# Performance work log

Hardware: AMD Instinct MI355X
Metric: run time of the kernel (lower is better)

Reference implementation:

```python
import jax, jax.numpy as jnp
import numpy as np

N_HEADS = 16
N_KV = 4
HEAD_DIM = 256
EPS = 1e-6

def _rotate_half(x):
    h = x.shape[-1] // 2
    return jnp.concatenate([-x[..., h:], x[..., :h]], axis=-1)

def _gemma_rmsnorm(x, w, eps=EPS):
    dt = x.dtype
    x32 = x.astype(jnp.float32)
    x32 = x32 * jax.lax.rsqrt(jnp.mean(x32 * x32, axis=-1, keepdims=True) + eps)
    return ((1.0 + w.astype(jnp.float32)) * x32).astype(dt)


def setup_inputs() -> dict:
    key = jax.random.key(0)
    ks = jax.random.split(key, 7)
    B, S, D = 2, 2048, 4096
    rotary_dim = 64
    x = jax.random.normal(ks[0], (B, S, D), jnp.float32)
    # realistic RoPE cache: [cos | sin], theta=10000
    inv_freq = 1.0 / (10000.0 ** (np.arange(0, rotary_dim, 2, dtype=np.float32) / rotary_dim))
    t = np.arange(S, dtype=np.float32)
    freqs = np.outer(t, inv_freq)                       # [S, rotary_dim/2]
    emb = np.concatenate([freqs, freqs], axis=-1)        # [S, rotary_dim]
    rope_cache = jnp.asarray(np.concatenate([np.cos(emb), np.sin(emb)], axis=-1))  # [S, 2*rotary_dim]
    sc = 0.02
    wq = jax.random.normal(ks[1], (N_HEADS * HEAD_DIM * 2, D), jnp.float32) * sc
    wk = jax.random.normal(ks[2], (N_KV * HEAD_DIM, D), jnp.float32) * sc
    wv = jax.random.normal(ks[3], (N_KV * HEAD_DIM, D), jnp.float32) * sc
    wo = jax.random.normal(ks[4], (D, N_HEADS * HEAD_DIM), jnp.float32) * sc
    q_norm_w = jnp.zeros((HEAD_DIM,), jnp.float32)
    k_norm_w = jnp.zeros((HEAD_DIM,), jnp.float32)
    return {"x": x, "rope_cache": rope_cache, "wq": wq, "wk": wk, "wv": wv,
            "wo": wo, "q_norm_w": q_norm_w, "k_norm_w": k_norm_w}


def reference(x, rope_cache, wq, wk, wv, wo, q_norm_w, k_norm_w):
    B, S, D = x.shape
    scale = HEAD_DIM ** -0.5
    # fused QKV-style projections
    qg = jnp.einsum('bsd,ed->bse', x, wq).reshape(B, S, N_HEADS, 2 * HEAD_DIM)
    q, gate = qg[..., :HEAD_DIM], qg[..., HEAD_DIM:]
    gate = gate.reshape(B, S, N_HEADS * HEAD_DIM)
    k = jnp.einsum('bsd,ed->bse', x, wk).reshape(B, S, N_KV, HEAD_DIM)
    v = jnp.einsum('bsd,ed->bse', x, wv).reshape(B, S, N_KV, HEAD_DIM)
    # QK RMSNorm (Gemma-style, zero-init weight)
    q = _gemma_rmsnorm(q, q_norm_w)
    k = _gemma_rmsnorm(k, k_norm_w)
    # partial RoPE on first rotary_dim dims
    rotary_dim = rope_cache.shape[-1] // 2
    rc = rope_cache[:S]
    cos = rc[None, :, None, :rotary_dim]
    sin = rc[None, :, None, rotary_dim:]
    q_rot = q[..., :rotary_dim] * cos + _rotate_half(q[..., :rotary_dim]) * sin
    k_rot = k[..., :rotary_dim] * cos + _rotate_half(k[..., :rotary_dim]) * sin
    q = jnp.concatenate([q_rot, q[..., rotary_dim:]], axis=-1)
    k = jnp.concatenate([k_rot, k[..., rotary_dim:]], axis=-1)
    # GQA: repeat kv heads
    rep = N_HEADS // N_KV
    k = jnp.repeat(k, rep, axis=2)  # [B,S,H,hd]
    v = jnp.repeat(v, rep, axis=2)
    # full (non-causal) SDPA
    scores = jnp.einsum('bqhd,bkhd->bhqk', q, k) * scale
    p = jax.nn.softmax(scores, axis=-1)
    y = jnp.einsum('bhqk,bkhd->bqhd', p, v).reshape(B, S, N_HEADS * HEAD_DIM)
    # sigmoid output gating
    y = y * jax.nn.sigmoid(gate)
    return jnp.einsum('bse,de->bsd', y, wo)
```

## Files before the change

### kernel.cpp

```cpp
#include <hip/hip_runtime.h>
#include <hip/hip_bf16.h>
#include <cstdint>
#include <cstddef>

typedef __bf16 bf16;
typedef __bf16 bf16x8 __attribute__((ext_vector_type(8)));
typedef __bf16 bf16x4 __attribute__((ext_vector_type(4)));
typedef float f32x4 __attribute__((ext_vector_type(4)));

#define MFMA16(a, b, c) __builtin_amdgcn_mfma_f32_16x16x32_bf16((a), (b), (c), 0, 0, 0)
#define GLL16(gp, lp) __builtin_amdgcn_global_load_lds( \
    (const __attribute__((address_space(1))) void*)(gp), \
    (__attribute__((address_space(3))) void*)(lp), 16, 0, 0)

#define LDS_FENCE() do { \
    __builtin_amdgcn_sched_barrier(0); \
    asm volatile("s_waitcnt lgkmcnt(0)" ::: "memory"); \
    __builtin_amdgcn_sched_barrier(0); \
  } while (0)

__device__ __forceinline__ bf16x8 cvt8(const float* f) {
  bf16x8 h;
  #pragma unroll
  for (int j = 0; j < 8; ++j) h[j] = (bf16)f[j];
  return h;
}

__device__ __forceinline__ bf16x8 ldb8(const bf16* p) {
  return *(const bf16x8*)p;
}
__device__ __forceinline__ bf16x8 ldb8(const float* p) {
  float f[8];
  *(f32x4*)&f[0] = *(const f32x4*)p;
  *(f32x4*)&f[4] = *(const f32x4*)(p + 4);
  return cvt8(f);
}

__global__ void write_val(float* o, float v) {
  if (threadIdx.x == 0 && blockIdx.x == 0) o[0] = v;
}

__global__ __launch_bounds__(256) void cvt_pass(
    const float* __restrict__ src, bf16* __restrict__ dst, size_t n8)
{
  for (size_t i = (size_t)blockIdx.x * 256 + threadIdx.x; i < n8;
       i += (size_t)gridDim.x * 256) {
    float f[8];
    *(f32x4*)&f[0] = *(const f32x4*)&src[i * 8];
    *(f32x4*)&f[4] = *(const f32x4*)&src[i * 8 + 4];
    *(bf16x8*)&dst[i * 8] = cvt8(f);
  }
}

template <typename CT>
__global__ __launch_bounds__(512, 2) void gemm256(
    const bf16* __restrict__ A,
    const bf16* __restrict__ B0, const bf16* __restrict__ B1, int nsplit,
    CT* __restrict__ C0, CT* __restrict__ C1,
    int K, size_t aBatch, size_t cBatch)
{
  __shared__ bf16 lds[4 * 16384];
  const int tid  = threadIdx.x;
  const int wave = tid >> 6, lane = tid & 63;
  const int g = lane >> 4, q = lane & 15;
  const int wm = wave >> 2, wn = wave & 3;
  const bool r0 = (int)blockIdx.x < nsplit;
  const bf16* Bw = r0 ? B0 : B1;
  CT* C = (r0 ? C0 : C1) + blockIdx.z * cBatch;
  const int bn = r0 ? blockIdx.x : blockIdx.x - nsplit;
  const int ldc = (r0 ? nsplit : ((int)gridDim.x - nsplit)) * 256;
  const size_t n0 = (size_t)bn * 256;
  const size_t m0 = (size_t)blockIdx.y * 256;
  const bf16* Ap = A + blockIdx.z * aBatch;

  const int srow = tid >> 2;
  const int scol = (((tid & 3) ^ (srow & 3)) << 3);
  const int NT = K >> 5;

  f32x4 acc[8][4] = {};

  auto STAGE_A = [&](int t) {
    const int k0 = t << 5;
    char* base = (char*)lds + (size_t)(t & 3) * 32768 + wave * 1024;
    #pragma unroll
    for (int i = 0; i < 2; ++i)
      GLL16(&Ap[(m0 + i * 128 + srow) * (size_t)K + k0 + scol],
            base + i * 8192);
  };
  auto STAGE_B = [&](int t) {
    const int k0 = t << 5;
    char* base = (char*)lds + (size_t)(t & 3) * 32768 + 16384 + wave * 1024;
    #pragma unroll
    for (int i = 0; i < 2; ++i)
      GLL16(&Bw[(n0 + i * 128 + srow) * (size_t)K + k0 + scol],
            base + i * 8192);
  };

  STAGE_A(0); STAGE_B(0);
  STAGE_A(1); STAGE_B(1);
  STAGE_A(2); STAGE_B(2);

  const int rsl = ((g ^ (q & 3)) << 3);

  for (int t = 0; t < NT; ++t) {
    asm volatile("s_waitcnt vmcnt(8)" ::: "memory");
    __builtin_amdgcn_sched_barrier(0);
    __builtin_amdgcn_s_barrier();
    const bf16* lA = lds + (size_t)(t & 3) * 16384;
    const bf16* lB = lA + 8192;

    bf16x8 bfr[4], af[4];
    #pragma unroll
    for (int fn = 0; fn < 4; ++fn)
      bfr[fn] = *(const bf16x8*)&lB[(wn * 64 + fn * 16 + q) * 32 + rsl];
    #pragma unroll
    for (int fm = 0; fm < 4; ++fm)
      af[fm] = *(const bf16x8*)&lA[(wm * 128 + fm * 16 + q) * 32 + rsl];
    if (t + 3 < NT) STAGE_A(t + 3);
    asm volatile("s_waitcnt lgkmcnt(0)" ::: "memory");
    __builtin_amdgcn_sched_barrier(0);
    __builtin_amdgcn_s_setprio(1);
    #pragma unroll
    for (int fm = 0; fm < 4; ++fm)
      #pragma unroll
      for (int fn = 0; fn < 4; ++fn)
        acc[fm][fn] = MFMA16(af[fm], bfr[fn], acc[fm][fn]);
    __builtin_amdgcn_s_setprio(0);
    __builtin_amdgcn_s_barrier();

    #pragma unroll
    for (int fm = 0; fm < 4; ++fm)
      af[fm] = *(const bf16x8*)&lA[(wm * 128 + (fm + 4) * 16 + q) * 32 + rsl];
    if (t + 3 < NT) STAGE_B(t + 3);
    asm volatile("s_waitcnt lgkmcnt(0)" ::: "memory");
    __builtin_amdgcn_sched_barrier(0);
    __builtin_amdgcn_s_setprio(1);
    #pragma unroll
    for (int fm = 0; fm < 4; ++fm)
      #pragma unroll
      for (int fn = 0; fn < 4; ++fn)
        acc[fm + 4][fn] = MFMA16(af[fm], bfr[fn], acc[fm + 4][fn]);
    __builtin_amdgcn_s_setprio(0);
  }

  #pragma unroll
  for (int fm = 0; fm < 8; ++fm)
    #pragma unroll
    for (int fn = 0; fn < 4; ++fn)
      #pragma unroll
      for (int r = 0; r < 4; ++r) {
        const size_t row = m0 + wm * 128 + fm * 16 + g * 4 + r;
        C[row * (size_t)ldc + n0 + wn * 64 + fn * 16 + q] = (CT)acc[fm][fn][r];
      }
}

template <typename CT, typename BT>
__global__ __launch_bounds__(256) void gemm_bf(
    const bf16* __restrict__ A,
    const BT* __restrict__ B0, const BT* __restrict__ B1, int nsplit,
    CT* __restrict__ C0, CT* __restrict__ C1,
    int K, size_t aBatch, size_t cBatch)
{
  constexpr int LDST = 72;
  __shared__ bf16 lA[128 * LDST];
  __shared__ bf16 lB[128 * LDST];
  const int tid  = threadIdx.x;
  const int wave = tid >> 6;
  const int lane = tid & 63;
  const int g = lane >> 4, q = lane & 15;
  const bool r0 = (int)blockIdx.x < nsplit;
  const BT* Bw = r0 ? B0 : B1;
  CT* C = (r0 ? C0 : C1) + blockIdx.z * cBatch;
  const int bn = r0 ? blockIdx.x : blockIdx.x - nsplit;
  const int ldc = (r0 ? nsplit : ((int)gridDim.x - nsplit)) * 128;
  const size_t n0 = (size_t)bn * 128;
  const size_t m0 = (size_t)blockIdx.y * 128;
  const bf16* Ap = A + blockIdx.z * aBatch;
  const int wm = wave >> 1, wn = wave & 1;
  const int sr = tid >> 3, sc8 = (tid & 7) << 3;

  f32x4 acc[4][4] = {};

  for (int k0 = 0; k0 < K; k0 += 64) {
    __syncthreads();
    #pragma unroll
    for (int i = 0; i < 4; ++i) {
      const int row = i * 32 + sr;
      *(bf16x8*)&lA[row * LDST + sc8] = ldb8(&Ap[(m0 + row) * (size_t)K + k0 + sc8]);
      *(bf16x8*)&lB[row * LDST + sc8] = ldb8(&Bw[(n0 + row) * (size_t)K + k0 + sc8]);
    }
    __syncthreads();
    #pragma unroll
    for (int kk = 0; kk < 2; ++kk) {
      bf16x8 af[4], bfr[4];
      #pragma unroll
      for (int f = 0; f < 4; ++f) {
        af[f]  = *(const bf16x8*)&lA[(wm * 64 + f * 16 + q) * LDST + kk * 32 + g * 8];
        bfr[f] = *(const bf16x8*)&lB[(wn * 64 + f * 16 + q) * LDST + kk * 32 + g * 8];
      }
      #pragma unroll
      for (int fm = 0; fm < 4; ++fm)
        #pragma unroll
        for (int fn = 0; fn < 4; ++fn)
          acc[fm][fn] = MFMA16(af[fm], bfr[fn], acc[fm][fn]);
    }
  }

  #pragma unroll
  for (int fm = 0; fm < 4; ++fm)
    #pragma unroll
    for (int fn = 0; fn < 4; ++fn)
      #pragma unroll
      for (int r = 0; r < 4; ++r) {
        const size_t row = m0 + wm * 64 + fm * 16 + g * 4 + r;
        C[row * (size_t)ldc + n0 + wn * 64 + fn * 16 + q] = (CT)acc[fm][fn][r];
      }
}

__global__ __launch_bounds__(256) void norm_rope_b(
    bf16* __restrict__ data, const float* __restrict__ w,
    const float* __restrict__ ropec, int hstride, int rowlen, int s_off)
{
  __shared__ float red[256];
  __shared__ float buf[256];
  const int t = threadIdx.x;
  const int m = blockIdx.x, h = blockIdx.y;
  const int s = (s_off + m) & 2047;

  bf16* p = data + (size_t)m * rowlen + h * hstride + t;
  const float x = (float)*p;
  red[t] = x * x;
  __syncthreads();
  for (int s2 = 128; s2 > 0; s2 >>= 1) {
    if (t < s2) red[t] += red[t + s2];
    __syncthreads();
  }
  const float rr = rsqrtf(red[0] * (1.0f / 256.0f) + 1e-6f);
  float xn = x * rr * (1.0f + w[t]);
  buf[t] = xn;
  __syncthreads();
  if (t < 64) {
    const float part = buf[(t < 32) ? t + 32 : t - 32];
    const float sgn  = (t < 32) ? -1.0f : 1.0f;
    const float* rc = ropec + (size_t)s * 128;
    xn = xn * rc[t] + sgn * part * rc[64 + t];
  }
  *p = (bf16)xn;
}

__global__ __launch_bounds__(256) void attn_b(
    const bf16* __restrict__ qg, const bf16* __restrict__ kb,
    const bf16* __restrict__ vb, bf16* __restrict__ yb)
{
  __shared__ bf16 lK[32 * 264];
  __shared__ bf16 lVt[256 * 40];
  __shared__ bf16 lP[4 * 16 * 40];
  const int tid  = threadIdx.x;
  const int wave = tid >> 6, lane = tid & 63;
  const int g = lane >> 4, qc = lane & 15;
  const int h = blockIdx.y, q0 = blockIdx.x * 64, kvh = h >> 2;
  const int qrow = q0 + wave * 16 + qc;

  bf16x8 qf[8];
  {
    const bf16* qp = qg + (size_t)qrow * 8192 + h * 512;
    #pragma unroll
    for (int kq = 0; kq < 8; ++kq)
      qf[kq] = *(const bf16x8*)&qp[kq * 32 + g * 8];
  }

  f32x4 o[16] = {};
  float mrow = -1e30f, lrow = 0.0f;
  const float scale = 0.0625f;
  const float L2E = 1.44269504f;
  const bf16* kbase = kb + kvh * 256;
  const bf16* vbase = vb + kvh * 256;
  const int vp = (tid & 15) * 2, vc = (tid >> 4) * 16;
  bf16* const pl = lP + wave * (16 * 40);

  for (int t0 = 0; t0 < 2048; t0 += 32) {
    bf16x8 ks[4];
    #pragma unroll
    for (int i = 0; i < 4; ++i) {
      const int v = i * 256 + tid;
      const int row = v >> 5, c8 = (v & 31) << 3;
      ks[i] = *(const bf16x8*)&kbase[(size_t)(t0 + row) * 1024 + c8];
    }
    bf16x8 v0a, v0b, v1a, v1b;
    {
      const bf16* p0 = vbase + (size_t)(t0 + vp) * 1024 + vc;
      v0a = *(const bf16x8*)(p0);
      v0b = *(const bf16x8*)(p0 + 8);
      v1a = *(const bf16x8*)(p0 + 1024);
      v1b = *(const bf16x8*)(p0 + 1032);
    }
    __syncthreads();
    #pragma unroll
    for (int i = 0; i < 4; ++i) {
      const int v = i * 256 + tid;
      const int row = v >> 5, c8 = (v & 31) << 3;
      *(bf16x8*)&lK[row * 264 + c8] = ks[i];
    }
    {
      unsigned* dst = (unsigned*)lVt;
      #pragma unroll
      for (int j = 0; j < 8; ++j) {
        const int o0 = (vc + j) * 20 + (vp >> 1);
        const int o1 = (vc + 8 + j) * 20 + (vp >> 1);
        dst[o0] = (unsigned)__builtin_bit_cast(unsigned short, (bf16)v0a[j]) |
                  ((unsigned)__builtin_bit_cast(unsigned short, (bf16)v1a[j]) << 16);
        dst[o1] = (unsigned)__builtin_bit_cast(unsigned short, (bf16)v0b[j]) |
                  ((unsigned)__builtin_bit_cast(unsigned short, (bf16)v1b[j]) << 16);
      }
    }
    __syncthreads();

    f32x4 st[2];
    #pragma unroll
    for (int half = 0; half < 2; ++half) {
      f32x4 s = {0.f, 0.f, 0.f, 0.f};
      #pragma unroll
      for (int kq = 0; kq < 8; ++kq) {
        const bf16x8 ka = *(const bf16x8*)
            &lK[(half * 16 + qc) * 264 + kq * 32 + g * 8];
        s = MFMA16(ka, qf[kq], s);
      }
      st[half] = s;
    }

    float pm = st[0][0];
    #pragma unroll
    for (int r = 1; r < 4; ++r) pm = fmaxf(pm, st[0][r]);
    #pragma unroll
    for (int r = 0; r < 4; ++r) pm = fmaxf(pm, st[1][r]);
    pm *= scale;
    pm = fmaxf(pm, __shfl_xor(pm, 16, 64));
    pm = fmaxf(pm, __shfl_xor(pm, 32, 64));

    const float mnew = fmaxf(mrow, pm);
    const float corr = exp2f((mrow - mnew) * L2E);
    lrow *= corr;
    #pragma unroll
    for (int f = 0; f < 16; ++f) {
      o[f][0] *= corr; o[f][1] *= corr; o[f][2] *= corr; o[f][3] *= corr;
    }
    mrow = mnew;

    float ladd = 0.0f;
    #pragma unroll
    for (int half = 0; half < 2; ++half) {
      bf16x4 pk;
      #pragma unroll
      for (int r = 0; r < 4; ++r) {
        const float pv = exp2f((st[half][r] * scale - mrow) * L2E);
        ladd += pv;
        pk[r] = (bf16)pv;
      }
      *(bf16x4*)&pl[qc * 40 + half * 16 + g * 4] = pk;
    }
    ladd += __shfl_xor(ladd, 16, 64);
    ladd += __shfl_xor(ladd, 32, 64);
    lrow += ladd;

    LDS_FENCE();

    const bf16x8 pb = *(const bf16x8*)&pl[qc * 40 + g * 8];
    #pragma unroll
    for (int fm = 0; fm < 16; ++fm) {
      const bf16x8 va = *(const bf16x8*)&lVt[(fm * 16 + qc) * 40 + g * 8];
      o[fm] = MFMA16(va, pb, o[fm]);
    }
  }

  const float inv = 1.0f / lrow;
  const bf16* gp = qg + (size_t)qrow * 8192 + h * 512 + 256;
  bf16* yp = yb + (size_t)qrow * 4096 + h * 256;
  #pragma unroll
  for (int fm = 0; fm < 16; ++fm) {
    const int d0 = fm * 16 + g * 4;
    bf16x4 ov;
    #pragma unroll
    for (int r = 0; r < 4; ++r) {
      const float gv = (float)gp[d0 + r];
      const float sig = 1.0f / (1.0f + exp2f(-gv * L2E));
      ov[r] = (bf16)(o[fm][r] * inv * sig);
    }
    *(bf16x4*)&yp[d0] = ov;
  }
}

extern "C" void kernel_launch(void* const* d_in, const int* in_sizes, int n_in,
                              void* d_out, int out_size, void* d_ws, size_t ws_size,
                              hipStream_t stream) {
  const float* x    = (const float*)d_in[0];
  const float* rope = (const float*)d_in[1];
  const float* wq   = (const float*)d_in[2];
  const float* wk   = (const float*)d_in[3];
  const float* wv   = (const float*)d_in[4];
  const float* wo   = (const float*)d_in[5];
  const float* qnw  = (const float*)d_in[6];
  const float* knw  = (const float*)d_in[7];
  float* out = (float*)d_out;

  if (out_size != 16777216) { write_val<<<1, 64, 0, stream>>>(out, 2000.0f); return; }
  const bool sizes_ok = (n_in == 8) &&
      in_sizes[0] == 16777216 && in_sizes[1] == 262144 &&
      in_sizes[2] == 33554432 && in_sizes[3] == 4194304 &&
      in_sizes[4] == 4194304  && in_sizes[5] == 16777216 &&
      in_sizes[6] == 256      && in_sizes[7] == 256;
  if (!sizes_ok) { write_val<<<1, 64, 0, stream>>>(out, 2500.0f); return; }

  const size_t XS  = 2048ull * 4096;
  const size_t KVS = 2048ull * 1024;
  const size_t WFIX = (33554432ull + 4194304 + 4194304 + 16777216) * 2;
  auto needT = [&](bool w, int nb, int CHv) -> size_t {
    return (w ? WFIX : 0)
         + (size_t)nb * XS * 2
         + (size_t)nb * KVS * 2 * 2
         + (size_t)CHv * 8192 * 2
         + (size_t)CHv * 4096 * 2;
  };
  bool useW = true; int nb = 2, CH = 2048;
  while (CH > 256 && needT(useW, nb, CH) > ws_size) CH >>= 1;
  if (needT(useW, nb, CH) > ws_size) {
    useW = false; CH = 2048;
    while (CH > 128 && needT(useW, nb, CH) > ws_size) CH >>= 1;
    if (needT(useW, nb, CH) > ws_size) {
      nb = 1; CH = 2048;
      while (CH > 128 && needT(useW, nb, CH) > ws_size) CH >>= 1;
    }
  }
  if (needT(useW, nb, CH) > ws_size) {
    write_val<<<1, 64, 0, stream>>>(out, 3000.0f);
    return;
  }

  char* ws = (char*)d_ws;
  bf16* wqb = nullptr; bf16* wkb = nullptr; bf16* wvb = nullptr; bf16* wob = nullptr;
  if (useW) {
    wqb = (bf16*)ws;               ws += 33554432ull * 2;
    wkb = (bf16*)ws;               ws += 4194304ull * 2;
    wvb = (bf16*)ws;               ws += 4194304ull * 2;
    wob = (bf16*)ws;               ws += 16777216ull * 2;
  }
  bf16* xb  = (bf16*)ws;           ws += (size_t)nb * XS * 2;
  bf16* kbb = (bf16*)ws;           ws += (size_t)nb * KVS * 2;
  bf16* vbb = (bf16*)ws;           ws += (size_t)nb * KVS * 2;
  bf16* qgc = (bf16*)ws;           ws += (size_t)CH * 8192 * 2;
  bf16* ycc = (bf16*)ws;

  if (useW) {
    cvt_pass<<<2048, 256, 0, stream>>>(wq, wqb, 33554432 / 8);
    cvt_pass<<<512,  256, 0, stream>>>(wk, wkb, 4194304 / 8);
    cvt_pass<<<512,  256, 0, stream>>>(wv, wvb, 4194304 / 8);
    cvt_pass<<<1024, 256, 0, stream>>>(wo, wob, 16777216 / 8);
  }

  if (nb == 2) {
    cvt_pass<<<2048, 256, 0, stream>>>(x, xb, 2 * XS / 8);
    if (useW)
      gemm256<bf16><<<dim3(8, 8, 2), 512, 0, stream>>>(
          xb, wkb, wvb, 4, kbb, vbb, 4096, XS, KVS);
    else
      gemm_bf<bf16, float><<<dim3(16, 16, 2), 256, 0, stream>>>(
          xb, wk, wv, 8, kbb, vbb, 4096, XS, KVS);
    norm_rope_b<<<dim3(4096, 4), 256, 0, stream>>>(kbb, knw, rope, 256, 1024, 0);
  }

  for (int b = 0; b < 2; ++b) {
    const int bi = (nb == 2) ? b : 0;
    if (nb == 1) {
      cvt_pass<<<2048, 256, 0, stream>>>(x + (size_t)b * XS, xb, XS / 8);
      if (useW)
        gemm256<bf16><<<dim3(8, 8, 1), 512, 0, stream>>>(
            xb, wkb, wvb, 4, kbb, vbb, 4096, 0, 0);
      else
        gemm_bf<bf16, float><<<dim3(16, 16, 1), 256, 0, stream>>>(
            xb, wk, wv, 8, kbb, vbb, 4096, 0, 0);
      norm_rope_b<<<dim3(2048, 4), 256, 0, stream>>>(kbb, knw, rope, 256, 1024, 0);
    }
    const bf16* xbb = xb + (size_t)bi * XS;
    bf16* kbbb = kbb + (size_t)bi * KVS;
    bf16* vbbb = vbb + (size_t)bi * KVS;
    for (int c = 0; c < 2048; c += CH) {
      if (useW)
        gemm256<bf16><<<dim3(32, CH / 256, 1), 512, 0, stream>>>(
            xbb + (size_t)c * 4096, wqb, wqb, 32, qgc, qgc, 4096, 0, 0);
      else
        gemm_bf<bf16, float><<<dim3(64, CH / 128, 1), 256, 0, stream>>>(
            xbb + (size_t)c * 4096, wq, wq, 64, qgc, qgc, 4096, 0, 0);
      norm_rope_b<<<dim3(CH, 16), 256, 0, stream>>>(qgc, qnw, rope, 512, 8192, c);
      attn_b<<<dim3(CH / 64, 16), 256, 0, stream>>>(qgc, kbbb, vbbb, ycc);
      float* outc = out + ((size_t)b * 2048 + c) * 4096;
      if (useW)
        gemm256<float><<<dim3(16, CH / 256, 1), 512, 0, stream>>>(
            ycc, wob, wob, 16, outc, outc, 4096, 0, 0);
      else
        gemm_bf<float, float><<<dim3(32, CH / 128, 1), 256, 0, stream>>>(
            ycc, wo, wo, 32, outc, outc, 4096, 0, 0);
    }
  }
}
```

Before: 1.004 ms.

## Fuse QKV GEMM, batch attention over both batches, warp-level norm/rope, swizzled K loads

Adds a full-workspace path that converts all inputs once, runs a single three-way GEMM producing K, V and Q/gate for both batches, then batched norm/rope, attention and output GEMM launches with no chunk loop. Norm/rope becomes one wavefront per head with shuffle reductions instead of LDS tree reductions. Attention loads K directly into a swizzled LDS layout via global_load_lds, raises wave priority around the MFMA loops, and skips the online-softmax rescale when the running max grows by at most 8. The lazy rescale changes numerics slightly, and the larger launches need more workspace.

```diff
diff --git a/kernel.cpp b/kernel.cpp
--- a/kernel.cpp
+++ b/kernel.cpp
@@ -53,22 +53,26 @@
 }
 
 template <typename CT>
-__global__ __launch_bounds__(512, 2) void gemm256(
+__global__ __launch_bounds__(512, 2) void gemm256_3(
     const bf16* __restrict__ A,
-    const bf16* __restrict__ B0, const bf16* __restrict__ B1, int nsplit,
-    CT* __restrict__ C0, CT* __restrict__ C1,
-    int K, size_t aBatch, size_t cBatch)
+    const bf16* __restrict__ B0, const bf16* __restrict__ B1,
+    const bf16* __restrict__ B2, int n1, int n2,
+    CT* __restrict__ C0, CT* __restrict__ C1, CT* __restrict__ C2,
+    int K, size_t aBatch, size_t cb0, size_t cb1, size_t cb2,
+    int ld0, int ld1, int ld2)
 {
   __shared__ bf16 lds[4 * 16384];
   const int tid  = threadIdx.x;
   const int wave = tid >> 6, lane = tid & 63;
   const int g = lane >> 4, q = lane & 15;
   const int wm = wave >> 2, wn = wave & 3;
-  const bool r0 = (int)blockIdx.x < nsplit;
-  const bf16* Bw = r0 ? B0 : B1;
-  CT* C = (r0 ? C0 : C1) + blockIdx.z * cBatch;
-  const int bn = r0 ? blockIdx.x : blockIdx.x - nsplit;
-  const int ldc = (r0 ? nsplit : ((int)gridDim.x - nsplit)) * 256;
+  const int bx = blockIdx.x;
+  const int r = (bx < n1) ? 0 : (bx < n2) ? 1 : 2;
+  const bf16* Bw = (r == 0) ? B0 : (r == 1) ? B1 : B2;
+  CT* C = ((r == 0) ? C0 : (r == 1) ? C1 : C2)
+          + blockIdx.z * ((r == 0) ? cb0 : (r == 1) ? cb1 : cb2);
+  const int bn = bx - ((r == 0) ? 0 : (r == 1) ? n1 : n2);
+  const int ldc = (r == 0) ? ld0 : (r == 1) ? ld1 : ld2;
   const size_t n0 = (size_t)bn * 256;
   const size_t m0 = (size_t)blockIdx.y * 256;
   const bf16* Ap = A + blockIdx.z * aBatch;
@@ -148,9 +152,9 @@
     #pragma unroll
     for (int fn = 0; fn < 4; ++fn)
       #pragma unroll
-      for (int r = 0; r < 4; ++r) {
-        const size_t row = m0 + wm * 128 + fm * 16 + g * 4 + r;
-        C[row * (size_t)ldc + n0 + wn * 64 + fn * 16 + q] = (CT)acc[fm][fn][r];
+      for (int rr = 0; rr < 4; ++rr) {
+        const size_t row = m0 + wm * 128 + fm * 16 + g * 4 + rr;
+        C[row * (size_t)ldc + n0 + wn * 64 + fn * 16 + q] = (CT)acc[fm][fn][rr];
       }
 }
 
@@ -217,53 +221,68 @@
       }
 }
 
-__global__ __launch_bounds__(256) void norm_rope_b(
+__global__ __launch_bounds__(256) void norm_rope_w(
     bf16* __restrict__ data, const float* __restrict__ w,
-    const float* __restrict__ ropec, int hstride, int rowlen, int s_off)
+    const float* __restrict__ ropec, int lnh, int hstride, int rowlen,
+    int s_off)
 {
-  __shared__ float red[256];
-  __shared__ float buf[256];
-  const int t = threadIdx.x;
-  const int m = blockIdx.x, h = blockIdx.y;
+  const int lane = threadIdx.x & 63;
+  const int wid  = blockIdx.x * 4 + (threadIdx.x >> 6);
+  const int m = wid >> lnh;
+  const int h = wid & ((1 << lnh) - 1);
   const int s = (s_off + m) & 2047;
 
-  bf16* p = data + (size_t)m * rowlen + h * hstride + t;
-  const float x = (float)*p;
-  red[t] = x * x;
-  __syncthreads();
-  for (int s2 = 128; s2 > 0; s2 >>= 1) {
-    if (t < s2) red[t] += red[t + s2];
-    __syncthreads();
-  }
-  const float rr = rsqrtf(red[0] * (1.0f / 256.0f) + 1e-6f);
-  float xn = x * rr * (1.0f + w[t]);
-  buf[t] = xn;
-  __syncthreads();
-  if (t < 64) {
-    const float part = buf[(t < 32) ? t + 32 : t - 32];
-    const float sgn  = (t < 32) ? -1.0f : 1.0f;
+  bf16* p = data + (size_t)m * rowlen + h * hstride + lane * 4;
+  const bf16x4 xv = *(const bf16x4*)p;
+  float x0 = (float)xv[0], x1 = (float)xv[1], x2 = (float)xv[2], x3 = (float)xv[3];
+  float ss = x0*x0 + x1*x1 + x2*x2 + x3*x3;
+  #pragma unroll
+  for (int d = 1; d < 64; d <<= 1) ss += __shfl_xor(ss, d, 64);
+  const float rr = rsqrtf(ss * (1.0f / 256.0f) + 1e-6f);
+  const f32x4 wv4 = *(const f32x4*)&w[lane * 4];
+  x0 *= rr * (1.0f + wv4[0]);
+  x1 *= rr * (1.0f + wv4[1]);
+  x2 *= rr * (1.0f + wv4[2]);
+  x3 *= rr * (1.0f + wv4[3]);
+
+  const float o0 = __shfl_xor(x0, 8, 64);
+  const float o1 = __shfl_xor(x1, 8, 64);
+  const float o2 = __shfl_xor(x2, 8, 64);
+  const float o3 = __shfl_xor(x3, 8, 64);
+  if (lane < 16) {
+    const int c0 = lane * 4;
     const float* rc = ropec + (size_t)s * 128;
-    xn = xn * rc[t] + sgn * part * rc[64 + t];
-  }
-  *p = (bf16)xn;
-}
-
-__global__ __launch_bounds__(256) void attn_b(
+    const float sgn = (lane < 8) ? -1.0f : 1.0f;
+    x0 = x0 * rc[c0]     + sgn * o0 * rc[64 + c0];
+    x1 = x1 * rc[c0 + 1] + sgn * o1 * rc[64 + c0 + 1];
+    x2 = x2 * rc[c0 + 2] + sgn * o2 * rc[64 + c0 + 2];
+    x3 = x3 * rc[c0 + 3] + sgn * o3 * rc[64 + c0 + 3];
+  }
+  bf16x4 ov; ov[0] = (bf16)x0; ov[1] = (bf16)x1; ov[2] = (bf16)x2; ov[3] = (bf16)x3;
+  *(bf16x4*)p = ov;
+}
+
+__global__ __launch_bounds__(256) void attn_b2(
     const bf16* __restrict__ qg, const bf16* __restrict__ kb,
-    const bf16* __restrict__ vb, bf16* __restrict__ yb)
+    const bf16* __restrict__ vb, bf16* __restrict__ yb,
+    size_t qgBatch, size_t kvBatch, size_t yBatch)
 {
-  __shared__ bf16 lK[32 * 264];
+  __shared__ bf16 lK[32 * 256];
   __shared__ bf16 lVt[256 * 40];
   __shared__ bf16 lP[4 * 16 * 40];
   const int tid  = threadIdx.x;
   const int wave = tid >> 6, lane = tid & 63;
   const int g = lane >> 4, qc = lane & 15;
   const int h = blockIdx.y, q0 = blockIdx.x * 64, kvh = h >> 2;
+  const int z = blockIdx.z;
+  const bf16* qgp = qg + z * qgBatch;
+  const bf16* kbase = kb + z * kvBatch + kvh * 256;
+  const bf16* vbase = vb + z * kvBatch + kvh * 256;
   const int qrow = q0 + wave * 16 + qc;
 
   bf16x8 qf[8];
   {
-    const bf16* qp = qg + (size_t)qrow * 8192 + h * 512;
+    const bf16* qp = qgp + (size_t)qrow * 8192 + h * 512;
     #pragma unroll
     for (int kq = 0; kq < 8; ++kq)
       qf[kq] = *(const bf16x8*)&qp[kq * 32 + g * 8];
@@ -273,19 +292,12 @@
   float mrow = -1e30f, lrow = 0.0f;
   const float scale = 0.0625f;
   const float L2E = 1.44269504f;
-  const bf16* kbase = kb + kvh * 256;
-  const bf16* vbase = vb + kvh * 256;
   const int vp = (tid & 15) * 2, vc = (tid >> 4) * 16;
   bf16* const pl = lP + wave * (16 * 40);
+  const int krw = wave * 2 + (lane >> 5);
+  const int ksl = lane & 31;
 
   for (int t0 = 0; t0 < 2048; t0 += 32) {
-    bf16x8 ks[4];
-    #pragma unroll
-    for (int i = 0; i < 4; ++i) {
-      const int v = i * 256 + tid;
-      const int row = v >> 5, c8 = (v & 31) << 3;
-      ks[i] = *(const bf16x8*)&kbase[(size_t)(t0 + row) * 1024 + c8];
-    }
     bf16x8 v0a, v0b, v1a, v1b;
     {
       const bf16* p0 = vbase + (size_t)(t0 + vp) * 1024 + vc;
@@ -297,9 +309,9 @@
     __syncthreads();
     #pragma unroll
     for (int i = 0; i < 4; ++i) {
-      const int v = i * 256 + tid;
-      const int row = v >> 5, c8 = (v & 31) << 3;
-      *(bf16x8*)&lK[row * 264 + c8] = ks[i];
+      const int row = i * 8 + krw;
+      GLL16(&kbase[(size_t)(t0 + row) * 1024 + ((ksl ^ (row & 7)) << 3)],
+            (char*)lK + i * 4096 + wave * 1024);
     }
     {
       unsigned* dst = (unsigned*)lVt;
@@ -319,12 +331,14 @@
     #pragma unroll
     for (int half = 0; half < 2; ++half) {
       f32x4 s = {0.f, 0.f, 0.f, 0.f};
+      __builtin_amdgcn_s_setprio(1);
       #pragma unroll
       for (int kq = 0; kq < 8; ++kq) {
         const bf16x8 ka = *(const bf16x8*)
-            &lK[(half * 16 + qc) * 264 + kq * 32 + g * 8];
+            &lK[(half * 16 + qc) * 256 + (((kq * 4 + g) ^ (qc & 7)) << 3)];
         s = MFMA16(ka, qf[kq], s);
       }
+      __builtin_amdgcn_s_setprio(0);
       st[half] = s;
     }
 
@@ -337,14 +351,16 @@
     pm = fmaxf(pm, __shfl_xor(pm, 16, 64));
     pm = fmaxf(pm, __shfl_xor(pm, 32, 64));
 
-    const float mnew = fmaxf(mrow, pm);
-    const float corr = exp2f((mrow - mnew) * L2E);
-    lrow *= corr;
-    #pragma unroll
-    for (int f = 0; f < 16; ++f) {
-      o[f][0] *= corr; o[f][1] *= corr; o[f][2] *= corr; o[f][3] *= corr;
-    }
-    mrow = mnew;
+    if (!__all(pm <= mrow + 8.0f)) {
+      const float mnew = fmaxf(mrow, pm);
+      const float corr = exp2f((mrow - mnew) * L2E);
+      lrow *= corr;
+      #pragma unroll
+      for (int f = 0; f < 16; ++f) {
+        o[f][0] *= corr; o[f][1] *= corr; o[f][2] *= corr; o[f][3] *= corr;
+      }
+      mrow = mnew;
+    }
 
     float ladd = 0.0f;
     #pragma unroll
@@ -365,16 +381,18 @@
     LDS_FENCE();
 
     const bf16x8 pb = *(const bf16x8*)&pl[qc * 40 + g * 8];
+    __builtin_amdgcn_s_setprio(1);
     #pragma unroll
     for (int fm = 0; fm < 16; ++fm) {
       const bf16x8 va = *(const bf16x8*)&lVt[(fm * 16 + qc) * 40 + g * 8];
       o[fm] = MFMA16(va, pb, o[fm]);
     }
+    __builtin_amdgcn_s_setprio(0);
   }
 
   const float inv = 1.0f / lrow;
-  const bf16* gp = qg + (size_t)qrow * 8192 + h * 512 + 256;
-  bf16* yp = yb + (size_t)qrow * 4096 + h * 256;
+  const bf16* gp = qgp + (size_t)qrow * 8192 + h * 512 + 256;
+  bf16* yp = yb + z * yBatch + (size_t)qrow * 4096 + h * 256;
   #pragma unroll
   for (int fm = 0; fm < 16; ++fm) {
     const int d0 = fm * 16 + g * 4;
@@ -412,14 +430,51 @@
 
   const size_t XS  = 2048ull * 4096;
   const size_t KVS = 2048ull * 1024;
+  const size_t QGS = 2048ull * 8192;
+  const size_t YS  = 2048ull * 4096;
   const size_t WFIX = (33554432ull + 4194304 + 4194304 + 16777216) * 2;
+
+  const size_t needFull = WFIX + 2 * XS * 2 + 4 * KVS * 2 + 2 * QGS * 2 + 2 * YS * 2;
   auto needT = [&](bool w, int nb, int CHv) -> size_t {
-    return (w ? WFIX : 0)
-         + (size_t)nb * XS * 2
-         + (size_t)nb * KVS * 2 * 2
-         + (size_t)CHv * 8192 * 2
-         + (size_t)CHv * 4096 * 2;
+    return (w ? WFIX : 0) + (size_t)nb * XS * 2 + (size_t)nb * KVS * 4
+         + (size_t)CHv * 8192 * 2 + (size_t)CHv * 4096 * 2;
   };
+
+  char* ws = (char*)d_ws;
+
+  if (needFull <= ws_size) {
+    bf16* wqb = (bf16*)ws;           ws += 33554432ull * 2;
+    bf16* wkb = (bf16*)ws;           ws += 4194304ull * 2;
+    bf16* wvb = (bf16*)ws;           ws += 4194304ull * 2;
+    bf16* wob = (bf16*)ws;           ws += 16777216ull * 2;
+    bf16* xb  = (bf16*)ws;           ws += 2 * XS * 2;
+    bf16* kbb = (bf16*)ws;           ws += 2 * KVS * 2;
+    bf16* vbb = (bf16*)ws;           ws += 2 * KVS * 2;
+    bf16* qgc = (bf16*)ws;           ws += 2 * QGS * 2;
+    bf16* ycc = (bf16*)ws;
+
+    cvt_pass<<<2048, 256, 0, stream>>>(wq, wqb, 33554432 / 8);
+    cvt_pass<<<512,  256, 0, stream>>>(wk, wkb, 4194304 / 8);
+    cvt_pass<<<512,  256, 0, stream>>>(wv, wvb, 4194304 / 8);
+    cvt_pass<<<1024, 256, 0, stream>>>(wo, wob, 16777216 / 8);
+    cvt_pass<<<2048, 256, 0, stream>>>(x, xb, 2 * XS / 8);
+
+    gemm256_3<bf16><<<dim3(40, 8, 2), 512, 0, stream>>>(
+        xb, wkb, wvb, wqb, 4, 8, kbb, vbb, qgc,
+        4096, XS, KVS, KVS, QGS, 1024, 1024, 8192);
+
+    norm_rope_w<<<4096,  256, 0, stream>>>(kbb, knw, rope, 2, 256, 1024, 0);
+    norm_rope_w<<<16384, 256, 0, stream>>>(qgc, qnw, rope, 4, 512, 8192, 0);
+
+    attn_b2<<<dim3(32, 16, 2), 256, 0, stream>>>(
+        qgc, kbb, vbb, ycc, QGS, KVS, YS);
+
+    gemm256_3<float><<<dim3(16, 8, 2), 512, 0, stream>>>(
+        ycc, wob, wob, wob, 16, 16, out, out, out,
+        4096, YS, YS, YS, YS, 4096, 4096, 4096);
+    return;
+  }
+
   bool useW = true; int nb = 2, CH = 2048;
   while (CH > 256 && needT(useW, nb, CH) > ws_size) CH >>= 1;
   if (needT(useW, nb, CH) > ws_size) {
@@ -435,7 +490,6 @@
     return;
   }
 
-  char* ws = (char*)d_ws;
   bf16* wqb = nullptr; bf16* wkb = nullptr; bf16* wvb = nullptr; bf16* wob = nullptr;
   if (useW) {
     wqb = (bf16*)ws;               ws += 33554432ull * 2;
@@ -459,12 +513,13 @@
   if (nb == 2) {
     cvt_pass<<<2048, 256, 0, stream>>>(x, xb, 2 * XS / 8);
     if (useW)
-      gemm256<bf16><<<dim3(8, 8, 2), 512, 0, stream>>>(
-          xb, wkb, wvb, 4, kbb, vbb, 4096, XS, KVS);
+      gemm256_3<bf16><<<dim3(8, 8, 2), 512, 0, stream>>>(
+          xb, wkb, wvb, wvb, 4, 8, kbb, vbb, vbb,
+          4096, XS, KVS, KVS, KVS, 1024, 1024, 1024);
     else
       gemm_bf<bf16, float><<<dim3(16, 16, 2), 256, 0, stream>>>(
           xb, wk, wv, 8, kbb, vbb, 4096, XS, KVS);
-    norm_rope_b<<<dim3(4096, 4), 256, 0, stream>>>(kbb, knw, rope, 256, 1024, 0);
+    norm_rope_w<<<4096, 256, 0, stream>>>(kbb, knw, rope, 2, 256, 1024, 0);
   }
 
   for (int b = 0; b < 2; ++b) {
@@ -472,29 +527,33 @@
     if (nb == 1) {
       cvt_pass<<<2048, 256, 0, stream>>>(x + (size_t)b * XS, xb, XS / 8);
       if (useW)
-        gemm256<bf16><<<dim3(8, 8, 1), 512, 0, stream>>>(
-            xb, wkb, wvb, 4, kbb, vbb, 4096, 0, 0);
+        gemm256_3<bf16><<<dim3(8, 8, 1), 512, 0, stream>>>(
+            xb, wkb, wvb, wvb, 4, 8, kbb, vbb, vbb,
+            4096, 0, 0, 0, 0, 1024, 1024, 1024);
       else
         gemm_bf<bf16, float><<<dim3(16, 16, 1), 256, 0, stream>>>(
             xb, wk, wv, 8, kbb, vbb, 4096, 0, 0);
-      norm_rope_b<<<dim3(2048, 4), 256, 0, stream>>>(kbb, knw, rope, 256, 1024, 0);
+      norm_rope_w<<<2048, 256, 0, stream>>>(kbb, knw, rope, 2, 256, 1024, 0);
     }
     const bf16* xbb = xb + (size_t)bi * XS;
     bf16* kbbb = kbb + (size_t)bi * KVS;
     bf16* vbbb = vbb + (size_t)bi * KVS;
     for (int c = 0; c < 2048; c += CH) {
       if (useW)
-        gemm256<bf16><<<dim3(32, CH / 256, 1), 512, 0, stream>>>(
-            xbb + (size_t)c * 4096, wqb, wqb, 32, qgc, qgc, 4096, 0, 0);
+        gemm256_3<bf16><<<dim3(32, CH / 256, 1), 512, 0, stream>>>(
+            xbb + (size_t)c * 4096, wqb, wqb, wqb, 32, 32, qgc, qgc, qgc,
+            4096, 0, 0, 0, 0, 8192, 8192, 8192);
       else
         gemm_bf<bf16, float><<<dim3(64, CH / 128, 1), 256, 0, stream>>>(
             xbb + (size_t)c * 4096, wq, wq, 64, qgc, qgc, 4096, 0, 0);
-      norm_rope_b<<<dim3(CH, 16), 256, 0, stream>>>(qgc, qnw, rope, 512, 8192, c);
-      attn_b<<<dim3(CH / 64, 16), 256, 0, stream>>>(qgc, kbbb, vbbb, ycc);
+      norm_rope_w<<<CH * 4, 256, 0, stream>>>(qgc, qnw, rope, 4, 512, 8192, c);
+      attn_b2<<<dim3(CH / 64, 16, 1), 256, 0, stream>>>(
+          qgc, kbbb, vbbb, ycc, 0, 0, 0);
       float* outc = out + ((size_t)b * 2048 + c) * 4096;
       if (useW)
-        gemm256<float><<<dim3(16, CH / 256, 1), 512, 0, stream>>>(
-            ycc, wob, wob, 16, outc, outc, 4096, 0, 0);
+        gemm256_3<float><<<dim3(16, CH / 256, 1), 512, 0, stream>>>(
+            ycc, wob, wob, wob, 16, 16, outc, outc, outc,
+            4096, 0, 0, 0, 0, 4096, 4096, 4096);
       else
         gemm_bf<float, float><<<dim3(32, CH / 128, 1), 256, 0, stream>>>(
             ycc, wo, wo, 32, outc, outc, 4096, 0, 0);
```

New measurement: 915.4 us. 1.1x faster.
